# Kernel tuning notes

Measured on AMD Instinct MI355X. Metric: run time of the kernel, lower is better.

## Reference

```python
import jax, jax.numpy as jnp
import numpy as np

WS = (7, 7)          # window size
DIM = 256            # projection_dim
HEADS = 8
B = 2048             # batch * num_windows
NW = 64              # windows per image (mask leading dim)


def _relative_position_index(ws):
    coords = np.stack(np.meshgrid(np.arange(ws[0]), np.arange(ws[1]), indexing='ij'))  # [2,h,w]
    flat = coords.reshape(2, -1)                                   # [2, h*w]
    rel = flat[:, :, None] - flat[:, None, :]                      # [2, N, N]
    rel = rel.transpose(1, 2, 0)                                   # [N, N, 2]
    rel[:, :, 0] += ws[0] - 1
    rel[:, :, 1] += ws[1] - 1
    idx = rel[:, :, 0] * (2 * ws[1] - 1) + rel[:, :, 1]            # [N, N]
    return idx.reshape(-1).astype(np.int32)                        # [N*N]


def setup_inputs() -> dict:
    key = jax.random.key(0)
    ks = jax.random.split(key, 6)
    N = WS[0] * WS[1]
    return {
        'x': jax.random.normal(ks[0], (B, N, DIM), jnp.float32),
        'mask': jax.random.normal(ks[1], (NW, N, N), jnp.float32),  # additive shift mask
        'qkv_w': jax.random.normal(ks[2], (DIM, 3 * DIM), jnp.float32) * (DIM ** -0.5),
        'qkv_b': jnp.zeros((3 * DIM,), jnp.float32),
        'proj_w': jax.random.normal(ks[3], (DIM, DIM), jnp.float32) * (DIM ** -0.5),
        'proj_b': jnp.zeros((DIM,), jnp.float32),
        'bias_table': jax.random.normal(ks[4], ((2 * WS[0] - 1) * (2 * WS[1] - 1), HEADS), jnp.float32) * 0.02,
        'rel_index': jnp.asarray(_relative_position_index(WS)),
    }


def reference(x, mask, qkv_w, qkv_b, proj_w, proj_b, bias_table, rel_index):
    Bn, N, C = x.shape
    hd = C // HEADS
    scale = hd ** -0.5
    qkv = x @ qkv_w + qkv_b                               # [B, N, 3C]
    qkv = qkv.reshape(Bn, N, 3, HEADS, hd).transpose(2, 0, 3, 1, 4)  # [3, B, H, N, hd]
    q, k, v = qkv[0], qkv[1], qkv[2]
    attn = jnp.einsum('bhnd,bhmd->bhnm', q * scale, k)    # [B, H, N, N]
    # gathered relative position bias: [N*N, H] -> [H, N, N]
    bias = bias_table[rel_index].reshape(N, N, HEADS).transpose(2, 0, 1)
    attn = attn + bias[None]
    nW = mask.shape[0]
    attn = attn.reshape(Bn // nW, nW, HEADS, N, N) + mask[None, :, None]
    attn = attn.reshape(Bn, HEADS, N, N)
    attn = jax.nn.softmax(attn, axis=-1)
    out = jnp.einsum('bhnm,bhmd->bhnd', attn, v)          # [B, H, N, hd]
    out = out.transpose(0, 2, 1, 3).reshape(Bn, N, C)
    return out @ proj_w + proj_b
```

## Files before the change

kernel.cpp:

```cpp
#include <hip/hip_runtime.h>


typedef __attribute__((ext_vector_type(8))) short v8s;
typedef __attribute__((ext_vector_type(4))) float v4f;

__device__ __forceinline__ unsigned short f2bf(float f) {
    union { float f; unsigned int i; } v; v.f = f;
    unsigned int x = v.i;
    return (unsigned short)((x + 0x7fffu + ((x >> 16) & 1u)) >> 16);
}

#define NW1 196608
#define NW2 65536
#define NB1 768
#define NCB 1605632
#define QSCALE_LOG2E 0.25503487f
#define LOG2E 1.4426950408889634f

__global__ void wattn_preproc(const float* __restrict__ qkv_w,
                              const float* __restrict__ qkv_b,
                              const float* __restrict__ proj_w,
                              const float* __restrict__ bias_table,
                              const float* __restrict__ mask,
                              const int* __restrict__ rel_index,
                              unsigned short* __restrict__ W1f,
                              unsigned short* __restrict__ W2f,
                              float* __restrict__ B1v,
                              float* __restrict__ CBf)
{
    const int idx = blockIdx.x * 256 + threadIdx.x;
    if (idx < NW1) {
        const int j = idx & 7, l = (idx >> 3) & 63, s = (idx >> 9) & 7, T = idx >> 12;
        const int k = s * 32 + (l >> 4) * 8 + j;
        const int n = T * 16 + (l & 15);
        const int hh = n / 96, sub = n % 96;
        const int col = (sub < 32) ? (hh * 32 + sub)
                      : (sub < 64) ? (256 + hh * 32 + (sub - 32))
                                   : (512 + hh * 32 + (sub - 64));
        float v = qkv_w[k * 768 + col];
        if (sub < 32) v *= QSCALE_LOG2E;
        W1f[idx] = f2bf(v);
    } else if (idx < NW1 + NW2) {
        const int t = idx - NW1;
        const int j = t & 7, l = (t >> 3) & 63, s = (t >> 9) & 7, T = t >> 12;
        const int k = s * 32 + (l >> 4) * 8 + j;
        const int n = T * 16 + (l & 15);
        W2f[t] = f2bf(proj_w[k * 256 + n]);
    } else if (idx < NW1 + NW2 + NB1) {
        const int n = idx - NW1 - NW2;
        const int hh = n / 96, sub = n % 96;
        const int col = (sub < 32) ? (hh * 32 + sub)
                      : (sub < 64) ? (256 + hh * 32 + (sub - 32))
                                   : (512 + hh * 32 + (sub - 64));
        float v = qkv_b[col];
        if (sub < 32) v *= QSCALE_LOG2E;
        B1v[n] = v;
    } else {
        const int t = idx - (NW1 + NW2 + NB1);
        if (t < NCB) {
            const int c = t & 63;
            const int rr = t >> 6;
            const int r = rr % 49;
            const int q2 = rr / 49;
            const int hh = q2 & 7;
            const int w = q2 >> 3;
            float v;
            if (c < 49) {
                const int ri = rel_index[r * 49 + c];
                v = (bias_table[ri * 8 + hh] + mask[(w * 49 + r) * 49 + c]) * LOG2E;
            } else {
                v = -1e30f;
            }
            CBf[t] = v;
        }
    }
}

__global__ __launch_bounds__(256, 2)
void wattn_main(const float* __restrict__ x,
                const unsigned short* __restrict__ W1f,
                const float* __restrict__ B1v,
                const float* __restrict__ CB,
                const unsigned short* __restrict__ W2f,
                const float* __restrict__ proj_b,
                float* __restrict__ out)
{
    __shared__ __align__(16) unsigned short xs[49 * 136];
    __shared__ __align__(16) unsigned short qs[49 * 40];
    __shared__ __align__(16) unsigned short ks[49 * 40];
    __shared__ __align__(16) unsigned short Vs[32 * 72];
    __shared__ __align__(16) unsigned short Ps[49 * 72];
    __shared__ __align__(16) unsigned short Os[49 * 264];

    const int tid  = threadIdx.x;
    const int wave = tid >> 6;
    const int lane = tid & 63;
    const int quad = lane >> 4;
    const int l15  = lane & 15;
    const int b    = blockIdx.x;
    const int widx = b & 63;
    const float* xw = x + (long)b * 49 * 256;
    const v4f zero4 = {0.0f, 0.0f, 0.0f, 0.0f};

    for (int i = tid; i < 32 * 15; i += 256) { const int d = i / 15, c = 49 + i % 15; Vs[d * 72 + c] = 0; }

    int arow[4];
    #pragma unroll
    for (int mt = 0; mt < 4; ++mt) {
        int m = mt * 16 + l15; if (m > 48) m = 48;
        arow[mt] = m * 136 + quad * 8;
    }

    #pragma unroll 1
    for (int p = 0; p < 2; ++p) {
        v4f acc[6][4];
        #pragma unroll
        for (int i = 0; i < 6; ++i)
            #pragma unroll
            for (int mt = 0; mt < 4; ++mt) acc[i][mt] = zero4;

        const int T0 = p * 24 + wave * 6;
        const unsigned short* bb = W1f + T0 * 4096 + lane * 8;

        #pragma unroll 1
        for (int ch = 0; ch < 2; ++ch) {
            __syncthreads();
            for (int i = tid; i < 1568; i += 256) {
                const int r = i >> 5, cq = i & 31;
                const float4 v = *reinterpret_cast<const float4*>(xw + r * 256 + ch * 128 + cq * 4);
                ushort4 o;
                o.x = f2bf(v.x); o.y = f2bf(v.y); o.z = f2bf(v.z); o.w = f2bf(v.w);
                *reinterpret_cast<ushort4*>(&xs[r * 136 + cq * 4]) = o;
            }
            __syncthreads();
            #pragma unroll
            for (int s = 0; s < 4; ++s) {
                v8s afr[4];
                #pragma unroll
                for (int mt = 0; mt < 4; ++mt)
                    afr[mt] = *reinterpret_cast<const v8s*>(&xs[arow[mt] + s * 32]);
                v8s bfr[6];
                #pragma unroll
                for (int i = 0; i < 6; ++i)
                    bfr[i] = *reinterpret_cast<const v8s*>(bb + i * 4096 + (ch * 4 + s) * 512);
                #pragma unroll
                for (int i = 0; i < 6; ++i)
                    #pragma unroll
                    for (int mt = 0; mt < 4; ++mt)
                        acc[i][mt] = __builtin_amdgcn_mfma_f32_16x16x32_bf16(afr[mt], bfr[i], acc[i][mt], 0, 0, 0);
            }
        }
        #pragma unroll
        for (int i = 0; i < 6; ++i) {
            const float bv = B1v[(T0 + i) * 16 + l15];
            #pragma unroll
            for (int mt = 0; mt < 4; ++mt) {
                acc[i][mt].x += bv; acc[i][mt].y += bv; acc[i][mt].z += bv; acc[i][mt].w += bv;
            }
        }

        for (int hh = 0; hh < 4; ++hh) {
            __syncthreads();
            if (wave == hh) {
                #pragma unroll
                for (int i = 0; i < 6; ++i) {
                    #pragma unroll
                    for (int mt = 0; mt < 4; ++mt) {
                        const int m0 = mt * 16 + quad * 4;
                        float vv[4] = {acc[i][mt].x, acc[i][mt].y, acc[i][mt].z, acc[i][mt].w};
                        if (i < 2) {
                            const int c = i * 16 + l15;
                            #pragma unroll
                            for (int r = 0; r < 4; ++r)
                                if (m0 + r < 49) qs[(m0 + r) * 40 + c] = f2bf(vv[r]);
                        } else if (i < 4) {
                            const int c = (i - 2) * 16 + l15;
                            #pragma unroll
                            for (int r = 0; r < 4; ++r)
                                if (m0 + r < 49) ks[(m0 + r) * 40 + c] = f2bf(vv[r]);
                        } else {
                            const int d = (i - 4) * 16 + l15;
                            if (mt < 3) {
                                ushort4 pk;
                                pk.x = f2bf(vv[0]); pk.y = f2bf(vv[1]);
                                pk.z = f2bf(vv[2]); pk.w = f2bf(vv[3]);
                                *reinterpret_cast<ushort4*>(&Vs[d * 72 + m0]) = pk;
                            } else if (quad == 0) {
                                Vs[d * 72 + 48] = f2bf(vv[0]);
                            }
                        }
                    }
                }
            }
            __syncthreads();

            const int h = p * 4 + hh;

            int aqr = wave * 16 + l15; if (aqr > 48) aqr = 48;
            const v8s aq = *reinterpret_cast<const v8s*>(&qs[aqr * 40 + quad * 8]);
            v4f sacc[4];
            #pragma unroll
            for (int nt = 0; nt < 4; ++nt) {
                int bkr = nt * 16 + l15; if (bkr > 48) bkr = 48;
                const v8s bk = *reinterpret_cast<const v8s*>(&ks[bkr * 40 + quad * 8]);
                sacc[nt] = __builtin_amdgcn_mfma_f32_16x16x32_bf16(aq, bk, zero4, 0, 0, 0);
            }

            const float* cbb = CB + (((long)widx * 8 + h) * 49) * 64;
            float pout[4][4];
            #pragma unroll
            for (int r = 0; r < 4; ++r) {
                const int m = wave * 16 + quad * 4 + r;
                const int mc = m > 48 ? 48 : m;
                float s0 = sacc[0][r] + cbb[mc * 64 + l15];
                float s1 = sacc[1][r] + cbb[mc * 64 + 16 + l15];
                float s2 = sacc[2][r] + cbb[mc * 64 + 32 + l15];
                float s3 = sacc[3][r] + cbb[mc * 64 + 48 + l15];
                float mx = fmaxf(fmaxf(s0, s1), fmaxf(s2, s3));
                #pragma unroll
                for (int off = 1; off < 16; off <<= 1) mx = fmaxf(mx, __shfl_xor(mx, off, 16));
                const float e0 = __builtin_exp2f(s0 - mx);
                const float e1 = __builtin_exp2f(s1 - mx);
                const float e2 = __builtin_exp2f(s2 - mx);
                const float e3 = __builtin_exp2f(s3 - mx);
                float sm = (e0 + e1) + (e2 + e3);
                #pragma unroll
                for (int off = 1; off < 16; off <<= 1) sm += __shfl_xor(sm, off, 16);
                const float rs = __builtin_amdgcn_rcpf(sm);
                pout[r][0] = e0 * rs; pout[r][1] = e1 * rs;
                pout[r][2] = e2 * rs; pout[r][3] = e3 * rs;
            }
            #pragma unroll
            for (int r = 0; r < 4; ++r) {
                const int m = wave * 16 + quad * 4 + r;
                if (m < 49) {
                    #pragma unroll
                    for (int nt = 0; nt < 4; ++nt)
                        Ps[m * 72 + nt * 16 + l15] = f2bf(pout[r][nt]);
                }
            }
            __syncthreads();

            int mrc = wave * 16 + l15; if (mrc > 48) mrc = 48;
            v4f oacc[2] = {zero4, zero4};
            #pragma unroll
            for (int kt = 0; kt < 2; ++kt) {
                const v8s ap = *reinterpret_cast<const v8s*>(&Ps[mrc * 72 + kt * 32 + quad * 8]);
                #pragma unroll
                for (int n2 = 0; n2 < 2; ++n2) {
                    const v8s bv = *reinterpret_cast<const v8s*>(&Vs[(n2 * 16 + l15) * 72 + kt * 32 + quad * 8]);
                    oacc[n2] = __builtin_amdgcn_mfma_f32_16x16x32_bf16(ap, bv, oacc[n2], 0, 0, 0);
                }
            }
            #pragma unroll
            for (int n2 = 0; n2 < 2; ++n2) {
                const int c = h * 32 + n2 * 16 + l15;
                #pragma unroll
                for (int r = 0; r < 4; ++r) {
                    const int m = wave * 16 + quad * 4 + r;
                    if (m < 49) Os[m * 264 + c] = f2bf(oacc[n2][r]);
                }
            }
        }
    }

    __syncthreads();

    v4f pacc[4][4];
    #pragma unroll
    for (int i = 0; i < 4; ++i)
        #pragma unroll
        for (int mt = 0; mt < 4; ++mt) pacc[i][mt] = zero4;

    int orow[4];
    #pragma unroll
    for (int mt = 0; mt < 4; ++mt) {
        int m = mt * 16 + l15; if (m > 48) m = 48;
        orow[mt] = m * 264 + quad * 8;
    }
    const unsigned short* wb = W2f + (wave * 4) * 4096 + lane * 8;

    #pragma unroll
    for (int s = 0; s < 8; ++s) {
        v8s afr[4];
        #pragma unroll
        for (int mt = 0; mt < 4; ++mt)
            afr[mt] = *reinterpret_cast<const v8s*>(&Os[orow[mt] + s * 32]);
        #pragma unroll
        for (int i = 0; i < 4; ++i) {
            const v8s bfp = *reinterpret_cast<const v8s*>(wb + i * 4096 + s * 512);
            #pragma unroll
            for (int mt = 0; mt < 4; ++mt)
                pacc[i][mt] = __builtin_amdgcn_mfma_f32_16x16x32_bf16(afr[mt], bfp, pacc[i][mt], 0, 0, 0);
        }
    }

    #pragma unroll
    for (int i = 0; i < 4; ++i) {
        const int c = (wave * 4 + i) * 16 + l15;
        const float pb = proj_b[c];
        #pragma unroll
        for (int mt = 0; mt < 4; ++mt) {
            #pragma unroll
            for (int r = 0; r < 4; ++r) {
                const int m = mt * 16 + quad * 4 + r;
                if (m < 49) out[((long)b * 49 + m) * 256 + c] = pacc[i][mt][r] + pb;
            }
        }
    }
}

extern "C" void kernel_launch(void* const* d_in, const int* in_sizes, int n_in,
                              void* d_out, int out_size, void* d_ws, size_t ws_size,
                              hipStream_t stream)
{
    const float* x          = (const float*)d_in[0];
    const float* mask       = (const float*)d_in[1];
    const float* qkv_w      = (const float*)d_in[2];
    const float* qkv_b      = (const float*)d_in[3];
    const float* proj_w     = (const float*)d_in[4];
    const float* proj_b     = (const float*)d_in[5];
    const float* bias_table = (const float*)d_in[6];
    const int*   rel_index  = (const int*)d_in[7];
    float* out = (float*)d_out;

    char* ws = (char*)d_ws;
    unsigned short* W1f = (unsigned short*)(ws);
    unsigned short* W2f = (unsigned short*)(ws + 393216);
    float*          B1v = (float*)(ws + 524288);
    float*          CBf = (float*)(ws + 527360);

    wattn_preproc<<<7299, 256, 0, stream>>>(qkv_w, qkv_b, proj_w, bias_table, mask,
                                            rel_index, W1f, W2f, B1v, CBf);
    wattn_main<<<2048, 256, 0, stream>>>(x, W1f, B1v, CBf, W2f, proj_b, out);
}
```

Before: 363.4 us.

## Process two heads per pass across wave pairs and fuse projection per head

Restructures the main kernel so that each pass computes QKV for two heads. Each pair of waves handles one head's attention, instead of four serialized single-head rounds where only one wave wrote Q/K/V. The full x tile is converted to bf16 once up front rather than in two chunks per pass. The output projection now accumulates per head pair inside the loop, reusing the P buffer as the O tile, which drops the separate Os buffer and the trailing projection phase. The intent is to remove idle waves and many __syncthreads barriers. The cost is a larger xs buffer and doubled per-head scratch buffers, which changes LDS use and occupancy.

```diff
diff --git a/kernel.cpp b/kernel.cpp
--- a/kernel.cpp
+++ b/kernel.cpp
@@ -16,6 +16,10 @@
 #define NCB 1605632
 #define QSCALE_LOG2E 0.25503487f
 #define LOG2E 1.4426950408889634f
+
+#define QS_H 1960
+#define VS_H 2304
+#define PS_H 3528
 
 __global__ void wattn_preproc(const float* __restrict__ qkv_w,
                               const float* __restrict__ qkv_b,
@@ -85,12 +89,11 @@
                 const float* __restrict__ proj_b,
                 float* __restrict__ out)
 {
-    __shared__ __align__(16) unsigned short xs[49 * 136];
-    __shared__ __align__(16) unsigned short qs[49 * 40];
-    __shared__ __align__(16) unsigned short ks[49 * 40];
-    __shared__ __align__(16) unsigned short Vs[32 * 72];
-    __shared__ __align__(16) unsigned short Ps[49 * 72];
-    __shared__ __align__(16) unsigned short Os[49 * 264];
+    __shared__ __align__(16) unsigned short xs[49 * 264];
+    __shared__ __align__(16) unsigned short qs[2 * QS_H];
+    __shared__ __align__(16) unsigned short ks[2 * QS_H];
+    __shared__ __align__(16) unsigned short Vs[2 * VS_H];
+    __shared__ __align__(16) unsigned short Ps[2 * PS_H];
 
     const int tid  = threadIdx.x;
     const int wave = tid >> 6;
@@ -102,120 +105,138 @@
     const float* xw = x + (long)b * 49 * 256;
     const v4f zero4 = {0.0f, 0.0f, 0.0f, 0.0f};
 
-    for (int i = tid; i < 32 * 15; i += 256) { const int d = i / 15, c = 49 + i % 15; Vs[d * 72 + c] = 0; }
+    const int hh01 = wave >> 1;
+    const int u0   = (wave & 1) * 3;
+    const int mb   = (wave & 1) * 2;
+
+    for (int i = tid; i < 960; i += 256) {
+        const int hd2 = i / 480, rem = i % 480;
+        Vs[hd2 * VS_H + (rem / 15) * 72 + 49 + rem % 15] = 0;
+    }
+    for (int i = tid; i < 49 * 64; i += 256) {
+        const int r = i >> 6, cq = i & 63;
+        const float4 v = *reinterpret_cast<const float4*>(xw + r * 256 + cq * 4);
+        ushort4 o;
+        o.x = f2bf(v.x); o.y = f2bf(v.y); o.z = f2bf(v.z); o.w = f2bf(v.w);
+        *reinterpret_cast<ushort4*>(&xs[r * 264 + cq * 4]) = o;
+    }
+    __syncthreads();
 
     int arow[4];
     #pragma unroll
     for (int mt = 0; mt < 4; ++mt) {
         int m = mt * 16 + l15; if (m > 48) m = 48;
-        arow[mt] = m * 136 + quad * 8;
-    }
+        arow[mt] = m * 264 + quad * 8;
+    }
+
+    v4f pacc[4][4];
+    #pragma unroll
+    for (int i = 0; i < 4; ++i)
+        #pragma unroll
+        for (int mt = 0; mt < 4; ++mt) pacc[i][mt] = zero4;
+
+    unsigned short* qb = qs + hh01 * QS_H;
+    unsigned short* kb = ks + hh01 * QS_H;
+    unsigned short* Vb = Vs + hh01 * VS_H;
+    unsigned short* Pb = Ps + hh01 * PS_H;
 
     #pragma unroll 1
-    for (int p = 0; p < 2; ++p) {
-        v4f acc[6][4];
-        #pragma unroll
-        for (int i = 0; i < 6; ++i)
+    for (int p = 0; p < 4; ++p) {
+        v4f acc[3][4];
+        #pragma unroll
+        for (int i = 0; i < 3; ++i)
             #pragma unroll
             for (int mt = 0; mt < 4; ++mt) acc[i][mt] = zero4;
 
-        const int T0 = p * 24 + wave * 6;
-        const unsigned short* bb = W1f + T0 * 4096 + lane * 8;
-
-        #pragma unroll 1
-        for (int ch = 0; ch < 2; ++ch) {
-            __syncthreads();
-            for (int i = tid; i < 1568; i += 256) {
-                const int r = i >> 5, cq = i & 31;
-                const float4 v = *reinterpret_cast<const float4*>(xw + r * 256 + ch * 128 + cq * 4);
-                ushort4 o;
-                o.x = f2bf(v.x); o.y = f2bf(v.y); o.z = f2bf(v.z); o.w = f2bf(v.w);
-                *reinterpret_cast<ushort4*>(&xs[r * 136 + cq * 4]) = o;
-            }
-            __syncthreads();
-            #pragma unroll
-            for (int s = 0; s < 4; ++s) {
-                v8s afr[4];
+        const int G0 = p * 12 + wave * 3;
+        const unsigned short* bb = W1f + G0 * 4096 + lane * 8;
+
+        #pragma unroll
+        for (int s = 0; s < 8; ++s) {
+            v8s afr[4];
+            #pragma unroll
+            for (int mt = 0; mt < 4; ++mt)
+                afr[mt] = *reinterpret_cast<const v8s*>(&xs[arow[mt] + s * 32]);
+            v8s bfr[3];
+            #pragma unroll
+            for (int i = 0; i < 3; ++i)
+                bfr[i] = *reinterpret_cast<const v8s*>(bb + i * 4096 + s * 512);
+            #pragma unroll
+            for (int i = 0; i < 3; ++i)
                 #pragma unroll
                 for (int mt = 0; mt < 4; ++mt)
-                    afr[mt] = *reinterpret_cast<const v8s*>(&xs[arow[mt] + s * 32]);
-                v8s bfr[6];
-                #pragma unroll
-                for (int i = 0; i < 6; ++i)
-                    bfr[i] = *reinterpret_cast<const v8s*>(bb + i * 4096 + (ch * 4 + s) * 512);
-                #pragma unroll
-                for (int i = 0; i < 6; ++i)
-                    #pragma unroll
-                    for (int mt = 0; mt < 4; ++mt)
-                        acc[i][mt] = __builtin_amdgcn_mfma_f32_16x16x32_bf16(afr[mt], bfr[i], acc[i][mt], 0, 0, 0);
-            }
-        }
-        #pragma unroll
-        for (int i = 0; i < 6; ++i) {
-            const float bv = B1v[(T0 + i) * 16 + l15];
+                    acc[i][mt] = __builtin_amdgcn_mfma_f32_16x16x32_bf16(afr[mt], bfr[i], acc[i][mt], 0, 0, 0);
+        }
+        #pragma unroll
+        for (int i = 0; i < 3; ++i) {
+            const float bv = B1v[(G0 + i) * 16 + l15];
             #pragma unroll
             for (int mt = 0; mt < 4; ++mt) {
                 acc[i][mt].x += bv; acc[i][mt].y += bv; acc[i][mt].z += bv; acc[i][mt].w += bv;
             }
         }
 
-        for (int hh = 0; hh < 4; ++hh) {
-            __syncthreads();
-            if (wave == hh) {
-                #pragma unroll
-                for (int i = 0; i < 6; ++i) {
+        #pragma unroll
+        for (int i = 0; i < 3; ++i) {
+            const int u = u0 + i;
+            #pragma unroll
+            for (int mt = 0; mt < 4; ++mt) {
+                const int m0 = mt * 16 + quad * 4;
+                float vv[4] = {acc[i][mt].x, acc[i][mt].y, acc[i][mt].z, acc[i][mt].w};
+                if (u < 2) {
+                    const int c = u * 16 + l15;
                     #pragma unroll
-                    for (int mt = 0; mt < 4; ++mt) {
-                        const int m0 = mt * 16 + quad * 4;
-                        float vv[4] = {acc[i][mt].x, acc[i][mt].y, acc[i][mt].z, acc[i][mt].w};
-                        if (i < 2) {
-                            const int c = i * 16 + l15;
-                            #pragma unroll
-                            for (int r = 0; r < 4; ++r)
-                                if (m0 + r < 49) qs[(m0 + r) * 40 + c] = f2bf(vv[r]);
-                        } else if (i < 4) {
-                            const int c = (i - 2) * 16 + l15;
-                            #pragma unroll
-                            for (int r = 0; r < 4; ++r)
-                                if (m0 + r < 49) ks[(m0 + r) * 40 + c] = f2bf(vv[r]);
-                        } else {
-                            const int d = (i - 4) * 16 + l15;
-                            if (mt < 3) {
-                                ushort4 pk;
-                                pk.x = f2bf(vv[0]); pk.y = f2bf(vv[1]);
-                                pk.z = f2bf(vv[2]); pk.w = f2bf(vv[3]);
-                                *reinterpret_cast<ushort4*>(&Vs[d * 72 + m0]) = pk;
-                            } else if (quad == 0) {
-                                Vs[d * 72 + 48] = f2bf(vv[0]);
-                            }
-                        }
+                    for (int r = 0; r < 4; ++r)
+                        if (m0 + r < 49) qb[(m0 + r) * 40 + c] = f2bf(vv[r]);
+                } else if (u < 4) {
+                    const int c = (u - 2) * 16 + l15;
+                    #pragma unroll
+                    for (int r = 0; r < 4; ++r)
+                        if (m0 + r < 49) kb[(m0 + r) * 40 + c] = f2bf(vv[r]);
+                } else {
+                    const int d = (u - 4) * 16 + l15;
+                    if (mt < 3) {
+                        ushort4 pk;
+                        pk.x = f2bf(vv[0]); pk.y = f2bf(vv[1]);
+                        pk.z = f2bf(vv[2]); pk.w = f2bf(vv[3]);
+                        *reinterpret_cast<ushort4*>(&Vb[d * 72 + m0]) = pk;
+                    } else if (quad == 0) {
+                        Vb[d * 72 + 48] = f2bf(vv[0]);
                     }
                 }
             }
-            __syncthreads();
-
-            const int h = p * 4 + hh;
-
-            int aqr = wave * 16 + l15; if (aqr > 48) aqr = 48;
-            const v8s aq = *reinterpret_cast<const v8s*>(&qs[aqr * 40 + quad * 8]);
-            v4f sacc[4];
-            #pragma unroll
-            for (int nt = 0; nt < 4; ++nt) {
-                int bkr = nt * 16 + l15; if (bkr > 48) bkr = 48;
-                const v8s bk = *reinterpret_cast<const v8s*>(&ks[bkr * 40 + quad * 8]);
-                sacc[nt] = __builtin_amdgcn_mfma_f32_16x16x32_bf16(aq, bk, zero4, 0, 0, 0);
-            }
-
-            const float* cbb = CB + (((long)widx * 8 + h) * 49) * 64;
-            float pout[4][4];
+        }
+        __syncthreads();
+
+        const int h = 2 * p + hh01;
+
+        v8s aq[2];
+        #pragma unroll
+        for (int mt2 = 0; mt2 < 2; ++mt2) {
+            int row = (mb + mt2) * 16 + l15; if (row > 48) row = 48;
+            aq[mt2] = *reinterpret_cast<const v8s*>(&qb[row * 40 + quad * 8]);
+        }
+        v4f sacc[2][4];
+        #pragma unroll
+        for (int nt = 0; nt < 4; ++nt) {
+            int kr = nt * 16 + l15; if (kr > 48) kr = 48;
+            const v8s bk = *reinterpret_cast<const v8s*>(&kb[kr * 40 + quad * 8]);
+            #pragma unroll
+            for (int mt2 = 0; mt2 < 2; ++mt2)
+                sacc[mt2][nt] = __builtin_amdgcn_mfma_f32_16x16x32_bf16(aq[mt2], bk, zero4, 0, 0, 0);
+        }
+
+        const float* cbb = CB + (((long)widx * 8 + h) * 49) * 64;
+        #pragma unroll
+        for (int mt2 = 0; mt2 < 2; ++mt2) {
             #pragma unroll
             for (int r = 0; r < 4; ++r) {
-                const int m = wave * 16 + quad * 4 + r;
+                const int m = (mb + mt2) * 16 + quad * 4 + r;
                 const int mc = m > 48 ? 48 : m;
-                float s0 = sacc[0][r] + cbb[mc * 64 + l15];
-                float s1 = sacc[1][r] + cbb[mc * 64 + 16 + l15];
-                float s2 = sacc[2][r] + cbb[mc * 64 + 32 + l15];
-                float s3 = sacc[3][r] + cbb[mc * 64 + 48 + l15];
+                float s0 = sacc[mt2][0][r] + cbb[mc * 64 + l15];
+                float s1 = sacc[mt2][1][r] + cbb[mc * 64 + 16 + l15];
+                float s2 = sacc[mt2][2][r] + cbb[mc * 64 + 32 + l15];
+                float s3 = sacc[mt2][3][r] + cbb[mc * 64 + 48 + l15];
                 float mx = fmaxf(fmaxf(s0, s1), fmaxf(s2, s3));
                 #pragma unroll
                 for (int off = 1; off < 16; off <<= 1) mx = fmaxf(mx, __shfl_xor(mx, off, 16));
@@ -227,71 +248,64 @@
                 #pragma unroll
                 for (int off = 1; off < 16; off <<= 1) sm += __shfl_xor(sm, off, 16);
                 const float rs = __builtin_amdgcn_rcpf(sm);
-                pout[r][0] = e0 * rs; pout[r][1] = e1 * rs;
-                pout[r][2] = e2 * rs; pout[r][3] = e3 * rs;
-            }
-            #pragma unroll
-            for (int r = 0; r < 4; ++r) {
-                const int m = wave * 16 + quad * 4 + r;
                 if (m < 49) {
-                    #pragma unroll
-                    for (int nt = 0; nt < 4; ++nt)
-                        Ps[m * 72 + nt * 16 + l15] = f2bf(pout[r][nt]);
+                    Pb[m * 72 + l15]      = f2bf(e0 * rs);
+                    Pb[m * 72 + 16 + l15] = f2bf(e1 * rs);
+                    Pb[m * 72 + 32 + l15] = f2bf(e2 * rs);
+                    Pb[m * 72 + 48 + l15] = f2bf(e3 * rs);
                 }
             }
-            __syncthreads();
-
-            int mrc = wave * 16 + l15; if (mrc > 48) mrc = 48;
-            v4f oacc[2] = {zero4, zero4};
-            #pragma unroll
-            for (int kt = 0; kt < 2; ++kt) {
-                const v8s ap = *reinterpret_cast<const v8s*>(&Ps[mrc * 72 + kt * 32 + quad * 8]);
-                #pragma unroll
-                for (int n2 = 0; n2 < 2; ++n2) {
-                    const v8s bv = *reinterpret_cast<const v8s*>(&Vs[(n2 * 16 + l15) * 72 + kt * 32 + quad * 8]);
-                    oacc[n2] = __builtin_amdgcn_mfma_f32_16x16x32_bf16(ap, bv, oacc[n2], 0, 0, 0);
+        }
+
+        int prow[2];
+        #pragma unroll
+        for (int mt2 = 0; mt2 < 2; ++mt2) {
+            int row = (mb + mt2) * 16 + l15; if (row > 48) row = 48;
+            prow[mt2] = row * 72;
+        }
+        v4f oacc[2][2] = {{zero4, zero4}, {zero4, zero4}};
+        #pragma unroll
+        for (int kt = 0; kt < 2; ++kt) {
+            v8s ap[2];
+            #pragma unroll
+            for (int mt2 = 0; mt2 < 2; ++mt2)
+                ap[mt2] = *reinterpret_cast<const v8s*>(&Pb[prow[mt2] + kt * 32 + quad * 8]);
+            #pragma unroll
+            for (int n2 = 0; n2 < 2; ++n2) {
+                const v8s bv = *reinterpret_cast<const v8s*>(&Vb[(n2 * 16 + l15) * 72 + kt * 32 + quad * 8]);
+                #pragma unroll
+                for (int mt2 = 0; mt2 < 2; ++mt2)
+                    oacc[mt2][n2] = __builtin_amdgcn_mfma_f32_16x16x32_bf16(ap[mt2], bv, oacc[mt2][n2], 0, 0, 0);
+            }
+        }
+        #pragma unroll
+        for (int mt2 = 0; mt2 < 2; ++mt2)
+            #pragma unroll
+            for (int n2 = 0; n2 < 2; ++n2)
+                #pragma unroll
+                for (int r = 0; r < 4; ++r) {
+                    const int m = (mb + mt2) * 16 + quad * 4 + r;
+                    if (m < 49) Pb[m * 72 + n2 * 16 + l15] = f2bf(oacc[mt2][n2][r]);
                 }
-            }
-            #pragma unroll
-            for (int n2 = 0; n2 < 2; ++n2) {
-                const int c = h * 32 + n2 * 16 + l15;
-                #pragma unroll
-                for (int r = 0; r < 4; ++r) {
-                    const int m = wave * 16 + quad * 4 + r;
-                    if (m < 49) Os[m * 264 + c] = f2bf(oacc[n2][r]);
-                }
-            }
-        }
-    }
-
-    __syncthreads();
-
-    v4f pacc[4][4];
-    #pragma unroll
-    for (int i = 0; i < 4; ++i)
-        #pragma unroll
-        for (int mt = 0; mt < 4; ++mt) pacc[i][mt] = zero4;
-
-    int orow[4];
-    #pragma unroll
-    for (int mt = 0; mt < 4; ++mt) {
-        int m = mt * 16 + l15; if (m > 48) m = 48;
-        orow[mt] = m * 264 + quad * 8;
-    }
-    const unsigned short* wb = W2f + (wave * 4) * 4096 + lane * 8;
-
-    #pragma unroll
-    for (int s = 0; s < 8; ++s) {
-        v8s afr[4];
-        #pragma unroll
-        for (int mt = 0; mt < 4; ++mt)
-            afr[mt] = *reinterpret_cast<const v8s*>(&Os[orow[mt] + s * 32]);
-        #pragma unroll
-        for (int i = 0; i < 4; ++i) {
-            const v8s bfp = *reinterpret_cast<const v8s*>(wb + i * 4096 + s * 512);
-            #pragma unroll
-            for (int mt = 0; mt < 4; ++mt)
-                pacc[i][mt] = __builtin_amdgcn_mfma_f32_16x16x32_bf16(afr[mt], bfp, pacc[i][mt], 0, 0, 0);
+        __syncthreads();
+
+        #pragma unroll
+        for (int hh = 0; hh < 2; ++hh) {
+            const unsigned short* Ob = Ps + hh * PS_H;
+            v8s oaf[4];
+            #pragma unroll
+            for (int mt = 0; mt < 4; ++mt) {
+                int row = mt * 16 + l15; if (row > 48) row = 48;
+                oaf[mt] = *reinterpret_cast<const v8s*>(&Ob[row * 72 + quad * 8]);
+            }
+            const int hg = 2 * p + hh;
+            #pragma unroll
+            for (int i = 0; i < 4; ++i) {
+                const v8s bfp = *reinterpret_cast<const v8s*>(W2f + (wave * 4 + i) * 4096 + hg * 512 + lane * 8);
+                #pragma unroll
+                for (int mt = 0; mt < 4; ++mt)
+                    pacc[i][mt] = __builtin_amdgcn_mfma_f32_16x16x32_bf16(oaf[mt], bfp, pacc[i][mt], 0, 0, 0);
+            }
         }
     }
 
```

Result: slower. 391.9 us (+7.8%).
